# Optimization experiments

Hardware: AMD Instinct MI355X
Metric: run time of the kernel (lower is better)

Reference implementation:

```python
import jax, jax.numpy as jnp
import numpy as np

BETA = 0.04
EPS_LOW = 0.2
EPS_HIGH = 0.2
KL_PERCENTILE = 0.2
TEMPERATURE = 1.0


def setup_inputs() -> dict:
    key = jax.random.key(0)
    k1, k2, k3, k4, k5, k6 = jax.random.split(key, 6)
    B, T, H, V = 8, 512, 1024, 32000
    scale = 0.02  # keep logits / log-ratios numerically sane
    return {
        "_input": jax.random.normal(k1, (B, T, H), jnp.float32) * scale,
        "lin_weight": jax.random.normal(k2, (V, H), jnp.float32) * scale,
        "selected_token_ids": jax.random.randint(k3, (B, T), 0, V, jnp.int32),
        "attention_mask": jnp.ones((B, T), jnp.float32),
        "advantages": jax.random.normal(k4, (B,), jnp.float32),
        "ref_input": jax.random.normal(k5, (B, T, H), jnp.float32) * scale,
        "ref_weight": jax.random.normal(k6, (V, H), jnp.float32) * scale,
    }


def _per_token_logps(x, w, ids):
    # x: [B,T,H], w: [V,H] -> log_softmax(logits/temp) gathered at ids -> [B,T]
    logits = jnp.einsum("bth,vh->btv", x, w) / TEMPERATURE
    logps = jax.nn.log_softmax(logits, axis=-1)
    return jnp.take_along_axis(logps, ids[..., None], axis=-1)[..., 0]


def _k3_percentile(log_p, log_q, percentile):
    # kthvalue over the whole batch of log_p (k-th smallest)
    flat = log_p.reshape(-1)
    n = flat.shape[0]
    k = max(1, int(n * percentile))
    threshold = jnp.sort(flat)[k - 1]
    mask = (log_p <= threshold).astype(log_p.dtype)
    log_ratio = log_p - log_q
    k3 = jnp.exp(log_ratio) - log_ratio - 1.0
    scale = 1.0 / percentile if percentile > 0 else 1.0
    return mask * k3 * scale


def reference(_input, lin_weight, selected_token_ids, attention_mask, advantages,
              ref_input, ref_weight):
    per_token_logps = _per_token_logps(_input, lin_weight, selected_token_ids)
    ref_per_token_logps = jax.lax.stop_gradient(
        _per_token_logps(ref_input, ref_weight, selected_token_ids))
    old_per_token_logps = jax.lax.stop_gradient(per_token_logps)

    # token-level importance sampling
    log_iw = per_token_logps - old_per_token_logps  # [B,T]
    coef_1 = jnp.exp(log_iw)
    coef_2 = jnp.clip(coef_1, 1.0 - EPS_LOW, 1.0 + EPS_HIGH)
    adv = advantages[:, None]  # [B,1]
    per_token_loss = -jnp.minimum(coef_1 * adv, coef_2 * adv)

    kl_div = _k3_percentile(ref_per_token_logps, per_token_logps, KL_PERCENTILE)
    per_token_loss = per_token_loss + BETA * kl_div

    # loss_type == 'dapo': normalize by total unmasked tokens (full batch)
    full_attention_mask = attention_mask
    normalizer = jnp.clip(full_attention_mask.sum(), 1.0, None)
    loss = (per_token_loss * attention_mask).sum() / normalizer

    kl_metric = (kl_div * attention_mask).sum() / jnp.clip(full_attention_mask.sum(), 1.0, None)
    is_clipped = ((coef_1 < 1.0 - EPS_LOW) & (adv < 0)) | ((coef_1 > 1.0 + EPS_HIGH) & (adv > 0))
    clip_ratio = (is_clipped.astype(jnp.float32) * attention_mask).sum() / jnp.clip(
        full_attention_mask.sum(), 1.0, None)
    return loss, kl_metric, clip_ratio
```

## Files before the change

kernel.cpp:

```cpp
#include <hip/hip_runtime.h>
#include <hip/hip_bf16.h>
#include <hip/hip_fp8.h>

typedef float f32x4  __attribute__((ext_vector_type(4)));
typedef float f32x16 __attribute__((ext_vector_type(16)));
typedef int   i32x4  __attribute__((ext_vector_type(4)));
typedef int   i32x8  __attribute__((ext_vector_type(8)));

#define NTOK 4096
#define TT   512
#define HH   1024
#define VV   32000

#define BM   128
#define BN   256
#define NKT  16

#define SC1  0x7F7F7F7F
#define INVS 0.000244140625f

#define GLOBAL_AS(p) ((const __attribute__((address_space(1))) void*)(const void*)(p))
#define LDS_AS(p)    ((__attribute__((address_space(3))) void*)(void*)(p))
#define BAR()   asm volatile("s_barrier" ::: "memory")
#define LGKM0() asm volatile("s_waitcnt lgkmcnt(0)" ::: "memory")
#define VM3()   asm volatile("s_waitcnt vmcnt(3)" ::: "memory")
#define SB0()   __builtin_amdgcn_sched_barrier(0)

__global__ __launch_bounds__(256)
void grpo_cvt_all(const float* __restrict__ X,  const float* __restrict__ W,
                  const float* __restrict__ Xr, const float* __restrict__ Wr,
                  unsigned char* __restrict__ Xq,  unsigned char* __restrict__ Wq,
                  unsigned char* __restrict__ Xrq, unsigned char* __restrict__ Wrq)
{
    const int nX8 = NTOK * HH / 8, nW8 = VV * HH / 8;
    const int b1 = nX8, b2 = nX8 + nW8, b3 = b2 + nX8;
    const int total = 2 * (nX8 + nW8);
    const int stride = gridDim.x * 256;
    for (int i = blockIdx.x * 256 + threadIdx.x; i < total; i += stride) {
        const float* s; unsigned char* d; int j;
        if      (i < b1) { s = X;  d = Xq;  j = i; }
        else if (i < b2) { s = W;  d = Wq;  j = i - b1; }
        else if (i < b3) { s = Xr; d = Xrq; j = i - b2; }
        else             { s = Wr; d = Wrq; j = i - b3; }
        f32x4 v0 = *(const f32x4*)(s + (size_t)j * 8);
        f32x4 v1 = *(const f32x4*)(s + (size_t)j * 8 + 4);
        union { unsigned char b[8]; unsigned long long u; } r;
#pragma unroll
        for (int e = 0; e < 4; ++e) r.b[e]     = __hip_fp8_e4m3(v0[e] * 64.0f).__x;
#pragma unroll
        for (int e = 0; e < 4; ++e) r.b[4 + e] = __hip_fp8_e4m3(v1[e] * 64.0f).__x;
        *(unsigned long long*)(d + (size_t)j * 8) = r.u;
    }
}

__global__ __launch_bounds__(512, 4)
void grpo_gemm_f8(const unsigned char* __restrict__ Xq,  const unsigned char* __restrict__ Wq,
                  const unsigned char* __restrict__ Xrq, const unsigned char* __restrict__ Wrq,
                  const int* __restrict__ ids,
                  float* __restrict__ S_p, float* __restrict__ SEL_p,
                  float* __restrict__ S_r, float* __restrict__ SEL_r)
{
    __shared__ int ldsw[12288];
    const int tid  = threadIdx.x;
    const int lane = tid & 63;
    const int wid  = tid >> 6;
    const int wr   = wid >> 2;
    const int wc   = wid & 3;
    const int l31  = lane & 31;
    const int hi   = lane >> 5;
    const int swz  = (l31 >> 1) & 3;
    const int s0   = ((2 * hi)     ^ swz) * 4;
    const int s1   = ((2 * hi + 1) ^ swz) * 4;

    const int zz = blockIdx.z;
    const unsigned char* Xs = zz ? Xrq : Xq;
    const unsigned char* Ws = zz ? Wrq : Wq;
    float* S   = zz ? S_r   : S_p;
    float* SEL = zz ? SEL_r : SEL_p;

    const int m0 = blockIdx.x * BM;
    const int n0 = blockIdx.y * BN;

    const int arow0 = (wr * 64 + l31) * 16;
    const int brow0 = (wc * 64 + l31) * 16;

    const int aRow  = tid >> 2;
    const int aSlot = ((tid & 3) ^ ((tid >> 3) & 3)) * 16;
    const unsigned char* gAb  = Xs + (size_t)(m0 + aRow) * HH + aSlot;
    const unsigned char* gBb0 = Ws + (size_t)(n0 + aRow) * HH + aSlot;
    const unsigned char* gBb1 = Ws + (size_t)(n0 + 128 + aRow) * HH + aSlot;
    char* ldsc = (char*)ldsw;
    char* dA   = ldsc + wid * 1024;
    char* dB0  = ldsc + 8192 + wid * 1024;
    char* dB1  = ldsc + 16384 + wid * 1024;

#define STAGE(BOFF, KC)                                                             \
    do {                                                                            \
        __builtin_amdgcn_global_load_lds(GLOBAL_AS(gAb  + (KC)), LDS_AS(dA  + (BOFF)), 16, 0, 0); \
        __builtin_amdgcn_global_load_lds(GLOBAL_AS(gBb0 + (KC)), LDS_AS(dB0 + (BOFF)), 16, 0, 0); \
        __builtin_amdgcn_global_load_lds(GLOBAL_AS(gBb1 + (KC)), LDS_AS(dB1 + (BOFF)), 16, 0, 0); \
    } while (0)

    f32x16 acc[2][2];
#pragma unroll
    for (int mi = 0; mi < 2; ++mi)
#pragma unroll
        for (int ni = 0; ni < 2; ++ni)
            acc[mi][ni] = (f32x16)0.0f;

    STAGE(0, 0);
    STAGE(24576, 64);
    VM3();
    BAR();

#define F8_BODY(BOFF, TNEXT)                                                        \
    {                                                                               \
        const int ab = (BOFF) / 4;                                                  \
        const int bb = (BOFF) / 4 + 2048;                                           \
        i32x4 a0l = *(const i32x4*)(ldsw + ab + arow0 + s0);                        \
        i32x4 a0h = *(const i32x4*)(ldsw + ab + arow0 + s1);                        \
        i32x4 a1l = *(const i32x4*)(ldsw + ab + arow0 + 512 + s0);                  \
        i32x4 a1h = *(const i32x4*)(ldsw + ab + arow0 + 512 + s1);                  \
        i32x4 b0l = *(const i32x4*)(ldsw + bb + brow0 + s0);                        \
        i32x4 b0h = *(const i32x4*)(ldsw + bb + brow0 + s1);                        \
        i32x4 b1l = *(const i32x4*)(ldsw + bb + brow0 + 512 + s0);                  \
        i32x4 b1h = *(const i32x4*)(ldsw + bb + brow0 + 512 + s1);                  \
        i32x8 a0 = __builtin_shufflevector(a0l, a0h, 0, 1, 2, 3, 4, 5, 6, 7);       \
        i32x8 a1 = __builtin_shufflevector(a1l, a1h, 0, 1, 2, 3, 4, 5, 6, 7);       \
        i32x8 b0 = __builtin_shufflevector(b0l, b0h, 0, 1, 2, 3, 4, 5, 6, 7);       \
        i32x8 b1 = __builtin_shufflevector(b1l, b1h, 0, 1, 2, 3, 4, 5, 6, 7);       \
        LGKM0(); BAR();                                                             \
        STAGE((((TNEXT) & 1) * 24576), (((TNEXT) & (NKT - 1)) * 64));               \
        SB0();                                                                      \
        __builtin_amdgcn_s_setprio(1);                                              \
        acc[0][0] = __builtin_amdgcn_mfma_scale_f32_32x32x64_f8f6f4(a0, b0, acc[0][0], 0, 0, 0, SC1, 0, SC1); \
        acc[0][1] = __builtin_amdgcn_mfma_scale_f32_32x32x64_f8f6f4(a0, b1, acc[0][1], 0, 0, 0, SC1, 0, SC1); \
        acc[1][0] = __builtin_amdgcn_mfma_scale_f32_32x32x64_f8f6f4(a1, b0, acc[1][0], 0, 0, 0, SC1, 0, SC1); \
        acc[1][1] = __builtin_amdgcn_mfma_scale_f32_32x32x64_f8f6f4(a1, b1, acc[1][1], 0, 0, 0, SC1, 0, SC1); \
        __builtin_amdgcn_s_setprio(0);                                              \
        VM3(); BAR();                                                               \
    }

#pragma unroll 1
    for (int t = 0; t < NKT; t += 2) {
        F8_BODY(0,     t + 2);
        F8_BODY(24576, t + 3);
    }

#pragma unroll
    for (int mi = 0; mi < 2; ++mi) {
#pragma unroll
        for (int rg = 0; rg < 16; ++rg) {
            const int row = m0 + wr * 64 + mi * 32 + (rg & 3) + 8 * (rg >> 2) + 4 * hi;
            const float v0 = acc[mi][0][rg] * INVS;
            const float v1 = acc[mi][1][rg] * INVS;
            float s = __expf(v0) + __expf(v1);
            s += __shfl_xor(s, 1, 64);
            s += __shfl_xor(s, 2, 64);
            s += __shfl_xor(s, 4, 64);
            s += __shfl_xor(s, 8, 64);
            s += __shfl_xor(s, 16, 64);
            if (l31 == 0) atomicAdd(&S[row], s);

            const int id = ids[row];
            const int c0 = n0 + wc * 64 + l31;
            if (id == c0)      SEL[row] = v0;
            if (id == c0 + 32) SEL[row] = v1;
        }
    }
#undef F8_BODY
#undef STAGE
}

__global__ void grpo_init(float* __restrict__ p)
{
    p[blockIdx.x * 1024 + threadIdx.x] = 0.f;
}

__global__ __launch_bounds__(1024)
void grpo_prep(const float* __restrict__ S_p, const float* __restrict__ S_r,
               float* __restrict__ lp_p, float* __restrict__ lp_r)
{
    int i = blockIdx.x * 1024 + threadIdx.x;
    lp_p[i] = lp_p[i] - logf(S_p[i]);
    lp_r[i] = lp_r[i] - logf(S_r[i]);
}

__global__ __launch_bounds__(64)
void grpo_thresh(const float* __restrict__ lp_r, float* __restrict__ thr)
{
    __shared__ float sh[NTOK];
    for (int i = threadIdx.x; i < NTOK; i += 64) sh[i] = lp_r[i];
    __syncthreads();
    const float v = sh[blockIdx.x * 64 + threadIdx.x];
    int lt = 0, eq = 0;
#pragma unroll 4
    for (int j = 0; j < NTOK; ++j) {
        float u = sh[j];
        lt += (u < v);
        eq += (u == v);
    }
    if (lt <= 818 && 818 < lt + eq) thr[0] = v;
}

__global__ __launch_bounds__(1024)
void grpo_final(const float* __restrict__ lp_p, const float* __restrict__ lp_r,
                const float* __restrict__ thr,
                const float* __restrict__ am, const float* __restrict__ adv,
                float* __restrict__ out)
{
    __shared__ double red[3][16];
    const int tid = threadIdx.x;
    const float t = thr[0];

    double s_loss = 0.0, s_kl = 0.0, s_am = 0.0;
    for (int i = tid; i < NTOK; i += 1024) {
        float a  = am[i];
        float pr = lp_r[i], pp = lp_p[i];
        float lr = pr - pp;
        float k3 = expf(lr) - lr - 1.0f;
        float kl = (pr <= t) ? k3 * 5.0f : 0.0f;
        float ad = adv[i / TT];
        float ptl = -ad + 0.04f * kl;
        s_loss += (double)(ptl * a);
        s_kl   += (double)(kl * a);
        s_am   += (double)a;
    }
#pragma unroll
    for (int off = 32; off; off >>= 1) {
        s_loss += __shfl_down(s_loss, off, 64);
        s_kl   += __shfl_down(s_kl,   off, 64);
        s_am   += __shfl_down(s_am,   off, 64);
    }
    const int wid = tid >> 6;
    if ((tid & 63) == 0) { red[0][wid] = s_loss; red[1][wid] = s_kl; red[2][wid] = s_am; }
    __syncthreads();
    if (tid == 0) {
        double L = 0, K = 0, A = 0;
        for (int w = 0; w < 16; ++w) { L += red[0][w]; K += red[1][w]; A += red[2][w]; }
        double norm = A < 1.0 ? 1.0 : A;
        out[0] = (float)(L / norm);
        out[1] = (float)(K / norm);
        out[2] = 0.0f;
    }
}

extern "C" void kernel_launch(void* const* d_in, const int* in_sizes, int n_in,
                              void* d_out, int out_size, void* d_ws, size_t ws_size,
                              hipStream_t stream)
{
    const float* X   = (const float*)d_in[0];
    const float* W   = (const float*)d_in[1];
    const int*   ids = (const int*)  d_in[2];
    const float* am  = (const float*)d_in[3];
    const float* adv = (const float*)d_in[4];
    const float* Xr  = (const float*)d_in[5];
    const float* Wr  = (const float*)d_in[6];
    float* out = (float*)d_out;

    float* S_p  = (float*)d_ws;
    float* S_r  = S_p + NTOK;
    float* lp_p = S_r + NTOK;
    float* lp_r = lp_p + NTOK;
    float* thr  = S_p;

    const size_t q_off = 65536;
    const size_t nX = (size_t)NTOK * HH, nW = (size_t)VV * HH;

    unsigned char* Xq  = (unsigned char*)d_ws + q_off;
    unsigned char* Wq  = Xq + nX;
    unsigned char* Xrq = Wq + nW;
    unsigned char* Wrq = Xrq + nX;

    hipLaunchKernelGGL(grpo_init, dim3(8), dim3(1024), 0, stream, S_p);

    hipLaunchKernelGGL(grpo_cvt_all, dim3(4096), dim3(256), 0, stream,
                       X, W, Xr, Wr, Xq, Wq, Xrq, Wrq);

    dim3 grid(NTOK / BM, VV / BN, 2);
    hipLaunchKernelGGL(grpo_gemm_f8, grid, dim3(512), 0, stream,
                       Xq, Wq, Xrq, Wrq, ids, S_p, lp_p, S_r, lp_r);

    hipLaunchKernelGGL(grpo_prep,   dim3(4),  dim3(1024), 0, stream, S_p, S_r, lp_p, lp_r);
    hipLaunchKernelGGL(grpo_thresh, dim3(64), dim3(64),   0, stream, lp_r, thr);
    hipLaunchKernelGGL(grpo_final,  dim3(1),  dim3(1024), 0, stream, lp_p, lp_r, thr, am, adv, out);
}
```

Measured before the change: 691.2 us.

## Enlarge FP8 GEMM tile to 256x256 with 128-byte K steps

Reworks the FP8 MFMA GEMM so each block computes a 256x256 tile instead of 128x256, and each K step loads 128 bytes instead of 64, so there are 8 K iterations. Each wave now holds a 4x2 grid of accumulators and issues 16 MFMAs per phase, with a new 8-way XOR LDS swizzle and double buffering in 128 KB of LDS. The aim is higher arithmetic intensity and fewer barriers per unit of work. In exchange, the large LDS footprint and accumulator register use lower occupancy, and the launch-bounds occupancy hint was removed.

```diff
diff --git a/kernel.cpp b/kernel.cpp
--- a/kernel.cpp
+++ b/kernel.cpp
@@ -12,9 +12,9 @@
 #define HH   1024
 #define VV   32000
 
-#define BM   128
+#define BM   256
 #define BN   256
-#define NKT  16
+#define NKT  8
 
 #define SC1  0x7F7F7F7F
 #define INVS 0.000244140625f
@@ -23,7 +23,8 @@
 #define LDS_AS(p)    ((__attribute__((address_space(3))) void*)(void*)(p))
 #define BAR()   asm volatile("s_barrier" ::: "memory")
 #define LGKM0() asm volatile("s_waitcnt lgkmcnt(0)" ::: "memory")
-#define VM3()   asm volatile("s_waitcnt vmcnt(3)" ::: "memory")
+#define VM8()   asm volatile("s_waitcnt vmcnt(8)" ::: "memory")
+#define VM0()   asm volatile("s_waitcnt vmcnt(0)" ::: "memory")
 #define SB0()   __builtin_amdgcn_sched_barrier(0)
 
 __global__ __launch_bounds__(256)
@@ -53,24 +54,93 @@
     }
 }
 
-__global__ __launch_bounds__(512, 4)
+template<int BOFF, int STG, int VMN>
+__device__ __forceinline__ void phaseF8(f32x16 (&acc)[4][2], const char* ldsc,
+                                        int arow, int brow,
+                                        int s00, int s01, int s10, int s11,
+                                        const unsigned char* gA, const unsigned char* gB,
+                                        char* dA, char* dB, int kc)
+{
+    const char* Ab = ldsc + BOFF + arow;
+    const char* Bb = ldsc + BOFF + 32768 + brow;
+
+    i32x8 a0[4], a1[4], b0[2], b1[2];
+#pragma unroll
+    for (int mi = 0; mi < 4; ++mi) {
+        i32x4 lo0 = *(const i32x4*)(Ab + mi * 4096 + s00);
+        i32x4 hi0 = *(const i32x4*)(Ab + mi * 4096 + s01);
+        i32x4 lo1 = *(const i32x4*)(Ab + mi * 4096 + s10);
+        i32x4 hi1 = *(const i32x4*)(Ab + mi * 4096 + s11);
+        a0[mi] = __builtin_shufflevector(lo0, hi0, 0, 1, 2, 3, 4, 5, 6, 7);
+        a1[mi] = __builtin_shufflevector(lo1, hi1, 0, 1, 2, 3, 4, 5, 6, 7);
+    }
+#pragma unroll
+    for (int ni = 0; ni < 2; ++ni) {
+        i32x4 lo0 = *(const i32x4*)(Bb + ni * 4096 + s00);
+        i32x4 hi0 = *(const i32x4*)(Bb + ni * 4096 + s01);
+        i32x4 lo1 = *(const i32x4*)(Bb + ni * 4096 + s10);
+        i32x4 hi1 = *(const i32x4*)(Bb + ni * 4096 + s11);
+        b0[ni] = __builtin_shufflevector(lo0, hi0, 0, 1, 2, 3, 4, 5, 6, 7);
+        b1[ni] = __builtin_shufflevector(lo1, hi1, 0, 1, 2, 3, 4, 5, 6, 7);
+    }
+
+    LGKM0();
+    BAR();
+    if (STG) {
+#pragma unroll
+        for (int i = 0; i < 4; ++i) {
+            __builtin_amdgcn_global_load_lds(GLOBAL_AS(gA + (size_t)i * 65536 + kc),
+                                             LDS_AS(dA + BOFF + i * 8192), 16, 0, 0);
+            __builtin_amdgcn_global_load_lds(GLOBAL_AS(gB + (size_t)i * 65536 + kc),
+                                             LDS_AS(dB + BOFF + i * 8192), 16, 0, 0);
+        }
+    }
+    SB0();
+
+    __builtin_amdgcn_s_setprio(1);
+#pragma unroll
+    for (int mi = 0; mi < 4; ++mi)
+#pragma unroll
+        for (int ni = 0; ni < 2; ++ni)
+            acc[mi][ni] = __builtin_amdgcn_mfma_scale_f32_32x32x64_f8f6f4(
+                a0[mi], b0[ni], acc[mi][ni], 0, 0, 0, SC1, 0, SC1);
+#pragma unroll
+    for (int mi = 0; mi < 4; ++mi)
+#pragma unroll
+        for (int ni = 0; ni < 2; ++ni)
+            acc[mi][ni] = __builtin_amdgcn_mfma_scale_f32_32x32x64_f8f6f4(
+                a1[mi], b1[ni], acc[mi][ni], 0, 0, 0, SC1, 0, SC1);
+    __builtin_amdgcn_s_setprio(0);
+
+    if (VMN == 8) VM8();
+    if (VMN == 0) VM0();
+    if (VMN >= 0) BAR();
+}
+
+__global__ __launch_bounds__(512)
 void grpo_gemm_f8(const unsigned char* __restrict__ Xq,  const unsigned char* __restrict__ Wq,
                   const unsigned char* __restrict__ Xrq, const unsigned char* __restrict__ Wrq,
                   const int* __restrict__ ids,
                   float* __restrict__ S_p, float* __restrict__ SEL_p,
                   float* __restrict__ S_r, float* __restrict__ SEL_r)
 {
-    __shared__ int ldsw[12288];
+    __shared__ char ldsc[131072];
+
     const int tid  = threadIdx.x;
     const int lane = tid & 63;
     const int wid  = tid >> 6;
     const int wr   = wid >> 2;
     const int wc   = wid & 3;
     const int l31  = lane & 31;
-    const int hi   = lane >> 5;
-    const int swz  = (l31 >> 1) & 3;
-    const int s0   = ((2 * hi)     ^ swz) * 4;
-    const int s1   = ((2 * hi + 1) ^ swz) * 4;
+    const int hf   = lane >> 5;
+    const int swz  = l31 & 7;
+
+    const int arow = (wr * 128 + l31) * 128;
+    const int brow = (wc * 64  + l31) * 128;
+    const int s00 = ((2 * hf)     ^ swz) * 16;
+    const int s01 = ((2 * hf + 1) ^ swz) * 16;
+    const int s10 = ((4 + 2 * hf)     ^ swz) * 16;
+    const int s11 = ((4 + 2 * hf + 1) ^ swz) * 16;
 
     const int zz = blockIdx.z;
     const unsigned char* Xs = zz ? Xrq : Xq;
@@ -81,77 +151,54 @@
     const int m0 = blockIdx.x * BM;
     const int n0 = blockIdx.y * BN;
 
-    const int arow0 = (wr * 64 + l31) * 16;
-    const int brow0 = (wc * 64 + l31) * 16;
-
-    const int aRow  = tid >> 2;
-    const int aSlot = ((tid & 3) ^ ((tid >> 3) & 3)) * 16;
-    const unsigned char* gAb  = Xs + (size_t)(m0 + aRow) * HH + aSlot;
-    const unsigned char* gBb0 = Ws + (size_t)(n0 + aRow) * HH + aSlot;
-    const unsigned char* gBb1 = Ws + (size_t)(n0 + 128 + aRow) * HH + aSlot;
-    char* ldsc = (char*)ldsw;
-    char* dA   = ldsc + wid * 1024;
-    char* dB0  = ldsc + 8192 + wid * 1024;
-    char* dB1  = ldsc + 16384 + wid * 1024;
-
-#define STAGE(BOFF, KC)                                                             \
-    do {                                                                            \
-        __builtin_amdgcn_global_load_lds(GLOBAL_AS(gAb  + (KC)), LDS_AS(dA  + (BOFF)), 16, 0, 0); \
-        __builtin_amdgcn_global_load_lds(GLOBAL_AS(gBb0 + (KC)), LDS_AS(dB0 + (BOFF)), 16, 0, 0); \
-        __builtin_amdgcn_global_load_lds(GLOBAL_AS(gBb1 + (KC)), LDS_AS(dB1 + (BOFF)), 16, 0, 0); \
-    } while (0)
-
-    f32x16 acc[2][2];
-#pragma unroll
-    for (int mi = 0; mi < 2; ++mi)
+    const int srow  = tid >> 3;
+    const int soff  = ((tid & 7) ^ ((tid >> 3) & 7)) * 16;
+    const unsigned char* gA = Xs + (size_t)(m0 + srow) * HH + soff;
+    const unsigned char* gB = Ws + (size_t)(n0 + srow) * HH + soff;
+    char* dA = ldsc + wid * 1024;
+    char* dB = ldsc + 32768 + wid * 1024;
+
+    f32x16 acc[4][2];
+#pragma unroll
+    for (int mi = 0; mi < 4; ++mi)
 #pragma unroll
         for (int ni = 0; ni < 2; ++ni)
             acc[mi][ni] = (f32x16)0.0f;
 
-    STAGE(0, 0);
-    STAGE(24576, 64);
-    VM3();
+#pragma unroll
+    for (int i = 0; i < 4; ++i) {
+        __builtin_amdgcn_global_load_lds(GLOBAL_AS(gA + (size_t)i * 65536),
+                                         LDS_AS(dA + i * 8192), 16, 0, 0);
+        __builtin_amdgcn_global_load_lds(GLOBAL_AS(gB + (size_t)i * 65536),
+                                         LDS_AS(dB + i * 8192), 16, 0, 0);
+    }
+#pragma unroll
+    for (int i = 0; i < 4; ++i) {
+        __builtin_amdgcn_global_load_lds(GLOBAL_AS(gA + (size_t)i * 65536 + 128),
+                                         LDS_AS(dA + 65536 + i * 8192), 16, 0, 0);
+        __builtin_amdgcn_global_load_lds(GLOBAL_AS(gB + (size_t)i * 65536 + 128),
+                                         LDS_AS(dB + 65536 + i * 8192), 16, 0, 0);
+    }
+    VM8();
     BAR();
 
-#define F8_BODY(BOFF, TNEXT)                                                        \
-    {                                                                               \
-        const int ab = (BOFF) / 4;                                                  \
-        const int bb = (BOFF) / 4 + 2048;                                           \
-        i32x4 a0l = *(const i32x4*)(ldsw + ab + arow0 + s0);                        \
-        i32x4 a0h = *(const i32x4*)(ldsw + ab + arow0 + s1);                        \
-        i32x4 a1l = *(const i32x4*)(ldsw + ab + arow0 + 512 + s0);                  \
-        i32x4 a1h = *(const i32x4*)(ldsw + ab + arow0 + 512 + s1);                  \
-        i32x4 b0l = *(const i32x4*)(ldsw + bb + brow0 + s0);                        \
-        i32x4 b0h = *(const i32x4*)(ldsw + bb + brow0 + s1);                        \
-        i32x4 b1l = *(const i32x4*)(ldsw + bb + brow0 + 512 + s0);                  \
-        i32x4 b1h = *(const i32x4*)(ldsw + bb + brow0 + 512 + s1);                  \
-        i32x8 a0 = __builtin_shufflevector(a0l, a0h, 0, 1, 2, 3, 4, 5, 6, 7);       \
-        i32x8 a1 = __builtin_shufflevector(a1l, a1h, 0, 1, 2, 3, 4, 5, 6, 7);       \
-        i32x8 b0 = __builtin_shufflevector(b0l, b0h, 0, 1, 2, 3, 4, 5, 6, 7);       \
-        i32x8 b1 = __builtin_shufflevector(b1l, b1h, 0, 1, 2, 3, 4, 5, 6, 7);       \
-        LGKM0(); BAR();                                                             \
-        STAGE((((TNEXT) & 1) * 24576), (((TNEXT) & (NKT - 1)) * 64));               \
-        SB0();                                                                      \
-        __builtin_amdgcn_s_setprio(1);                                              \
-        acc[0][0] = __builtin_amdgcn_mfma_scale_f32_32x32x64_f8f6f4(a0, b0, acc[0][0], 0, 0, 0, SC1, 0, SC1); \
-        acc[0][1] = __builtin_amdgcn_mfma_scale_f32_32x32x64_f8f6f4(a0, b1, acc[0][1], 0, 0, 0, SC1, 0, SC1); \
-        acc[1][0] = __builtin_amdgcn_mfma_scale_f32_32x32x64_f8f6f4(a1, b0, acc[1][0], 0, 0, 0, SC1, 0, SC1); \
-        acc[1][1] = __builtin_amdgcn_mfma_scale_f32_32x32x64_f8f6f4(a1, b1, acc[1][1], 0, 0, 0, SC1, 0, SC1); \
-        __builtin_amdgcn_s_setprio(0);                                              \
-        VM3(); BAR();                                                               \
-    }
-
 #pragma unroll 1
-    for (int t = 0; t < NKT; t += 2) {
-        F8_BODY(0,     t + 2);
-        F8_BODY(24576, t + 3);
-    }
-
-#pragma unroll
-    for (int mi = 0; mi < 2; ++mi) {
+    for (int it = 0; it < 3; ++it) {
+        phaseF8<0,     1, 8>(acc, ldsc, arow, brow, s00, s01, s10, s11,
+                             gA, gB, dA, dB, (2 * it + 2) * 128);
+        phaseF8<65536, 1, 8>(acc, ldsc, arow, brow, s00, s01, s10, s11,
+                             gA, gB, dA, dB, (2 * it + 3) * 128);
+    }
+    phaseF8<0,     0,  0>(acc, ldsc, arow, brow, s00, s01, s10, s11,
+                          gA, gB, dA, dB, 0);
+    phaseF8<65536, 0, -1>(acc, ldsc, arow, brow, s00, s01, s10, s11,
+                          gA, gB, dA, dB, 0);
+
+#pragma unroll
+    for (int mi = 0; mi < 4; ++mi) {
 #pragma unroll
         for (int rg = 0; rg < 16; ++rg) {
-            const int row = m0 + wr * 64 + mi * 32 + (rg & 3) + 8 * (rg >> 2) + 4 * hi;
+            const int row = m0 + wr * 128 + mi * 32 + (rg & 3) + 8 * (rg >> 2) + 4 * hf;
             const float v0 = acc[mi][0][rg] * INVS;
             const float v1 = acc[mi][1][rg] * INVS;
             float s = __expf(v0) + __expf(v1);
@@ -168,8 +215,6 @@
             if (id == c0 + 32) SEL[row] = v1;
         }
     }
-#undef F8_BODY
-#undef STAGE
 }
 
 __global__ void grpo_init(float* __restrict__ p)
```

Result: slower. 1.129 ms (+63.4%).
